# Performance work log

Hardware: AMD Instinct MI355X
Metric: run time of the kernel (lower is better)

Reference implementation:

```python
import jax, jax.numpy as jnp
import numpy as np

B, N_PER_G, H, K, A, GNN_STEPS = 64, 100, 64, 5, 50, 3
N = B * N_PER_G  # total nodes


def _lin(key, din, dout):
    s = 1.0 / np.sqrt(din)
    kw, kb = jax.random.split(key)
    w = jax.random.uniform(kw, (din, dout), minval=-s, maxval=s, dtype=jnp.float32)
    b = jax.random.uniform(kb, (dout,), minval=-s, maxval=s, dtype=jnp.float32)
    return w, b


def setup_inputs() -> dict:
    key = jax.random.key(0)
    ks = jax.random.split(key, 16)
    # complete graph (no self loops) per batch graph
    i, j = np.meshgrid(np.arange(N_PER_G), np.arange(N_PER_G), indexing="ij")
    m = i != j
    s0, d0 = i[m], j[m]  # [n*(n-1)]
    offs = (np.arange(B) * N_PER_G)[:, None]
    src = jnp.asarray((s0[None, :] + offs).reshape(-1), dtype=jnp.int32)
    dst = jnp.asarray((d0[None, :] + offs).reshape(-1), dtype=jnp.int32)
    E = src.shape[0]
    e_type = jax.random.uniform(ks[0], (E, 2), dtype=jnp.float32)
    d = jax.random.uniform(ks[1], (E, 1), dtype=jnp.float32)
    label = jax.nn.one_hot(jax.random.randint(ks[2], (N,), 0, K), K, dtype=jnp.float32)
    actions = jax.random.randint(ks[3], (B * A, 2), 0, N_PER_G)
    l1_w, l1_b = _lin(ks[4], K, H)
    l2_w, l2_b = _lin(ks[5], H, H)
    t3_w, t3_b = _lin(ks[6], H, H)
    t4_wf, t4_b = _lin(ks[7], 1, H)
    t5_wf, t5_b = _lin(ks[8], H, 1)
    t6_w, t6_b = _lin(ks[9], H, H)
    t7_1_w, t7_1_b = _lin(ks[10], H, H)
    t7_2_w, t7_2_b = _lin(ks[11], H, H)
    t9_1_w, t9_1_b = _lin(ks[12], H, H)
    t9_2_w, t9_2_b = _lin(ks[13], H, H)
    return dict(label=label, e_type=e_type, d=d,
                l1_w=l1_w, l1_b=l1_b, l2_w=l2_w, l2_b=l2_b,
                t3_w=t3_w, t3_b=t3_b, t4_w=t4_wf[0], t4_b=t4_b,
                t5_w=t5_wf[:, 0], t5_b=t5_b, t6_w=t6_w, t6_b=t6_b,
                t7_1_w=t7_1_w, t7_1_b=t7_1_b, t7_2_w=t7_2_w, t7_2_b=t7_2_b,
                t9_1_w=t9_1_w, t9_1_b=t9_1_b, t9_2_w=t9_2_w, t9_2_b=t9_2_b,
                src=src, dst=dst, actions=actions)


def reference(label, e_type, d, l1_w, l1_b, l2_w, l2_b, t3_w, t3_b, t4_w, t4_b,
              t5_w, t5_b, t6_w, t6_b, t7_1_w, t7_1_b, t7_2_w, t7_2_b,
              t9_1_w, t9_1_b, t9_2_w, t9_2_b, src, dst, actions):
    e1 = e_type[:, 0]
    # n1_hd = h[src]*e1, n1_d = d*e1; bmm(n1_hd^T, n1_d) == sum over in-edges of h[src]*e1^2*d
    w_e = (e1 * e1) * d[:, 0]                              # [E]
    s_e = d[:, 0] * e1                                     # per-edge n1_d scalar [E]
    # sum_deg relu(t4(n1_d)) as edge-parallel relu + scatter-add
    t4_edge = jax.nn.relu(s_e[:, None] * t4_w[None, :] + t4_b)   # [E,H]
    t4_sum = jax.ops.segment_sum(t4_edge, dst, num_segments=N)   # [N,H]
    base = label @ l1_w + l1_b + t4_sum @ t3_w + t3_b            # constant across gnn steps
    h = jnp.zeros((N, H), dtype=label.dtype)
    for _ in range(GNN_STEPS):
        n1_h = jax.ops.segment_sum(h[src] * w_e[:, None], dst, num_segments=N)  # [N,H]
        h = jax.nn.relu(base + n1_h @ l2_w + l2_b)
    # readout (forward_): graph mean -> t6 stem; per-action node-pair branch
    stem = h.reshape(B, N_PER_G, H).mean(axis=1) @ t6_w + t6_b    # [B,H]
    h2 = h @ t7_1_w + t7_1_b                                      # [N,H]
    offs = jnp.repeat(jnp.arange(B, dtype=actions.dtype) * N_PER_G, A)
    a = actions + offs[:, None]                                   # global node ids [B*A,2]
    ha = h2[a[:, 0]] + h2[a[:, 1]]                                # [B*A,H]
    u = jax.nn.relu(jax.nn.relu(ha) @ t7_2_w + t7_2_b) @ t9_2_w + t9_2_b
    g_branch = jax.nn.relu(stem) @ t9_1_w + t9_1_b                # [B,H]
    q = jax.nn.relu(g_branch[:, None, :] + u.reshape(B, A, H))    # [B,A,H]
    Q_sa = q.reshape(B * A, H) @ t5_w + t5_b[0]                   # [B*A]
    return Q_sa
```

## Files before the change

kernel.cpp:

```cpp
#include <hip/hip_runtime.h>

#define HD 64
#define NPG 100
#define NGRP 64
#define NACT 50
#define EPG 9900
#define HSTRIDE 409600
#define FLAGSTRIDE 4096
#define MAGICF 0x9E3779B9u

typedef const float* fcp;

#define ACC_CHUNK(CK)                                                         \
    for (int ib = 0; ib < 7; ++ib) {                                          \
        const float h0 = hs[((CK) * 28 + 4 * ib + 0) * HD + hh];              \
        const float h1 = hs[((CK) * 28 + 4 * ib + 1) * HD + hh];              \
        const float h2 = hs[((CK) * 28 + 4 * ib + 2) * HD + hh];              \
        const float h3 = hs[((CK) * 28 + 4 * ib + 3) * HD + hh];              \
        _Pragma("unroll")                                                     \
        for (int m = 0; m < 4; ++m) {                                         \
            const int jl = w + 8 * m;                                         \
            if (jl < 25) {                                                    \
                const float4 wv =                                             \
                    *(const float4*)&w_pad[jl * 112 + (CK) * 28 + 4 * ib];    \
                acc[m] += wv.x * h0 + wv.y * h1 + wv.z * h2 + wv.w * h3;      \
            }                                                                 \
        }                                                                     \
    }

__global__ __launch_bounds__(512)
void k_dqnet(fcp label, fcp e_type, fcp dvec,
             fcp l1_w, fcp l1_b, fcp l2_w, fcp l2_b,
             fcp t3_w, fcp t3_b, fcp t4_w, fcp t4_b,
             fcp t5_w, fcp t5_b, fcp t6_w, fcp t6_b,
             fcp t7_1_w, fcp t7_1_b, fcp t7_2_w, fcp t7_2_b,
             fcp t9_1_w, fcp t9_1_b, fcp t9_2_w, fcp t9_2_b,
             const int* __restrict__ actions,
             float* __restrict__ hstg, unsigned* __restrict__ flags,
             float* __restrict__ out)
{
    const int g  = blockIdx.x >> 2;
    const int c  = blockIdx.x & 3;
    const int j0 = c * 25;
    const int t  = threadIdx.x;
    const int hh = t & 63;
    const int w  = t >> 6;

    __shared__ __align__(16) float s_ld[2500];
    __shared__ __align__(16) float w_pad[25 * 112];
    __shared__ __align__(16) float hs[112 * HD];
    __shared__ __align__(16) float t4s[25 * HD];
    __shared__ __align__(16) float sh_l2w[HD * HD];
    __shared__ __align__(16) float sh_w71[HD * HD];
    __shared__ __align__(16) float sh_w72[HD * HD];
    __shared__ __align__(16) float sh_w92[HD * HD];
    __shared__ __align__(16) float awk[8 * HD];
    __shared__ float gbuf[HD];

    float l1r[5], lab[4][5];
    #pragma unroll
    for (int kk = 0; kk < 5; ++kk) l1r[kk] = l1_w[kk * HD + hh];
    #pragma unroll
    for (int m = 0; m < 4; ++m) {
        const int jl = w + 8 * m;
        #pragma unroll
        for (int kk = 0; kk < 5; ++kk)
            lab[m][kk] = (jl < 25) ? label[(g * NPG + j0 + jl) * 5 + kk] : 0.f;
    }
    const int acnt  = (c < 2) ? 13 : 12;
    const int abase = c * 12 + (c < 2 ? c : 2);
    int a0r[2], a1r[2];
    #pragma unroll
    for (int m = 0; m < 2; ++m) {
        const int al = w + 7 * m;
        a0r[m] = 0; a1r[m] = 0;
        if (w < 7 && al < acnt) {
            const int a = g * NACT + abase + al;
            a0r[m] = actions[a * 2 + 0];
            a1r[m] = actions[a * 2 + 1];
        }
        a0r[m] += 3 * (a0r[m] / 25);
        a1r[m] += 3 * (a1r[m] / 25);
    }

    for (int idx = t; idx < 768; idx += 512) {
        const int c2 = idx / 192, r = (idx % 192) / 64, ln = idx & 63;
        hs[(c2 * 28 + 25 + r) * HD + ln] = 0.f;
    }
    for (int idx = t; idx < 300; idx += 512) {
        const int jl = idx / 12, p = idx % 12;
        w_pad[jl * 112 + (p / 3) * 28 + 25 + (p % 3)] = 0.f;
    }

    const float2* et2 = (const float2*)e_type;
    const int ebase = g * EPG;
    for (int idx = t; idx < 2500; idx += 512) {
        const int i  = idx / 25;
        const int jl = idx - i * 25;
        const int j  = j0 + jl;
        float s = 0.f, wv = 0.f;
        if (i != j) {
            const int e = ebase + i * 99 + j - (j > i ? 1 : 0);
            const float e1 = et2[e].x;
            const float dd = dvec[e];
            s  = dd * e1;
            wv = e1 * e1 * dd;
        }
        s_ld[jl * 100 + i] = s;
        const int cb = i / 25;
        w_pad[jl * 112 + cb * 28 + (i - cb * 25)] = wv;
    }
    __syncthreads();

    const float w4  = t4_w[hh];
    const float b4  = t4_b[hh];
    const float rb4 = fmaxf(b4, 0.f);
    #pragma unroll
    for (int m = 0; m < 4; ++m) {
        const int jl = w + 8 * m;
        if (jl < 25) {
            float a0 = 0.f, a1 = 0.f, a2 = 0.f, a3 = 0.f;
            #pragma unroll 5
            for (int ib = 0; ib < 25; ++ib) {
                const float4 s4 = *(const float4*)&s_ld[jl * 100 + 4 * ib];
                a0 += fmaxf(s4.x * w4 + b4, 0.f);
                a1 += fmaxf(s4.y * w4 + b4, 0.f);
                a2 += fmaxf(s4.z * w4 + b4, 0.f);
                a3 += fmaxf(s4.w * w4 + b4, 0.f);
            }
            t4s[jl * HD + hh] = (a0 + a1) + (a2 + a3) - rb4;
        }
    }

    const float bb   = l1_b[hh] + t3_b[hh];
    const float l2bv = l2_b[hh];
    float basev[4];
    #pragma unroll
    for (int m = 0; m < 4; ++m) {
        float x = bb;
        #pragma unroll
        for (int kk = 0; kk < 5; ++kk) x += lab[m][kk] * l1r[kk];
        basev[m] = x;
    }
    for (int ib = 0; ib < 16; ++ib) {
        const float tw0 = t3_w[(4 * ib + 0) * HD + hh];
        const float tw1 = t3_w[(4 * ib + 1) * HD + hh];
        const float tw2 = t3_w[(4 * ib + 2) * HD + hh];
        const float tw3 = t3_w[(4 * ib + 3) * HD + hh];
        #pragma unroll
        for (int m = 0; m < 4; ++m) {
            const int jl = w + 8 * m;
            if (jl < 25) {
                const float4 x4 = *(const float4*)&t4s[jl * HD + 4 * ib];
                basev[m] += x4.x * tw0 + x4.y * tw1 + x4.z * tw2 + x4.w * tw3;
            }
        }
    }
    {
        #pragma unroll
        for (int m = 0; m < 4; ++m) {
            const int jl = w + 8 * m;
            if (jl < 25) {
                const float hv = fmaxf(basev[m] + l2bv, 0.f);
                hs[(c * 28 + jl) * HD + hh] = hv;
                __hip_atomic_store(hstg + (g * NPG + j0 + jl) * HD + hh, hv,
                                   __ATOMIC_RELAXED, __HIP_MEMORY_SCOPE_AGENT);
            }
        }
        asm volatile("s_waitcnt vmcnt(0)" ::: "memory");
        __syncthreads();
        if (t == 0)
            __hip_atomic_store(&flags[(g * 4 + c) * 16], MAGICF,
                               __ATOMIC_RELEASE, __HIP_MEMORY_SCOPE_AGENT);
    }

    {
        const float4* ls = (const float4*)l2_w;
        float4* ld = (float4*)sh_l2w;
        for (int idx = t; idx < 1024; idx += 512) ld[idx] = ls[idx];
        const float4* s71 = (const float4*)t7_1_w;
        float4* d71 = (float4*)sh_w71;
        for (int idx = t; idx < 1024; idx += 512) d71[idx] = s71[idx];
        const float4* s72 = (const float4*)t7_2_w;
        float4* d72 = (float4*)sh_w72;
        for (int idx = t; idx < 1024; idx += 512) d72[idx] = s72[idx];
        const float4* s92 = (const float4*)t9_2_w;
        float4* d92 = (float4*)sh_w92;
        for (int idx = t; idx < 1024; idx += 512) d92[idx] = s92[idx];
    }

    const int c1 = (c + 1) & 3, c2i = (c + 2) & 3, c3 = (c + 3) & 3;
    #pragma unroll 1
    for (int step = 0; step < 2; ++step) {
        const float* buf = hstg + step * HSTRIDE;
        unsigned* flg = flags + step * FLAGSTRIDE;
        float* bufn = hstg + (step + 1) * HSTRIDE;
        unsigned* flgn = flags + (step + 1) * FLAGSTRIDE;

        float acc[4];
        #pragma unroll
        for (int m = 0; m < 4; ++m) acc[m] = 0.f;

        ACC_CHUNK(c)

        if (t < 3) {
            const int cs = (c + 1 + t) & 3;
            while (__hip_atomic_load(&flg[(g * 4 + cs) * 16],
                                     __ATOMIC_RELAXED,
                                     __HIP_MEMORY_SCOPE_AGENT) != MAGICF)
                __builtin_amdgcn_s_sleep(1);
        }
        __syncthreads();

        const double* sb = (const double*)buf;
        const double* s1 = sb + (size_t)(g * NPG + c1 * 25) * 32;
        const double* s2 = sb + (size_t)(g * NPG + c2i * 25) * 32;
        const double* s3 = sb + (size_t)(g * NPG + c3 * 25) * 32;
        double* d1 = (double*)&hs[c1 * 28 * HD];
        double* d2 = (double*)&hs[c2i * 28 * HD];
        double* d3 = (double*)&hs[c3 * 28 * HD];
        const bool g2 = (t < 288);

        double a0 = __hip_atomic_load(s1 + t, __ATOMIC_RELAXED, __HIP_MEMORY_SCOPE_AGENT);
        double a1 = g2 ? __hip_atomic_load(s1 + 512 + t, __ATOMIC_RELAXED, __HIP_MEMORY_SCOPE_AGENT) : 0.0;
        double b0 = __hip_atomic_load(s2 + t, __ATOMIC_RELAXED, __HIP_MEMORY_SCOPE_AGENT);
        double b1 = g2 ? __hip_atomic_load(s2 + 512 + t, __ATOMIC_RELAXED, __HIP_MEMORY_SCOPE_AGENT) : 0.0;
        d1[t] = a0; if (g2) d1[512 + t] = a1;
        __syncthreads();
        double e0 = __hip_atomic_load(s3 + t, __ATOMIC_RELAXED, __HIP_MEMORY_SCOPE_AGENT);
        double e1 = g2 ? __hip_atomic_load(s3 + 512 + t, __ATOMIC_RELAXED, __HIP_MEMORY_SCOPE_AGENT) : 0.0;
        ACC_CHUNK(c1)
        d2[t] = b0; if (g2) d2[512 + t] = b1;
        __syncthreads();
        ACC_CHUNK(c2i)
        d3[t] = e0; if (g2) d3[512 + t] = e1;
        __syncthreads();
        ACC_CHUNK(c3)

        #pragma unroll
        for (int m = 0; m < 4; ++m) {
            const int jl = w + 8 * m;
            if (jl < 25) t4s[jl * HD + hh] = acc[m];
        }
        float v[4];
        #pragma unroll
        for (int m = 0; m < 4; ++m) v[m] = basev[m] + l2bv;
        for (int ib = 0; ib < 16; ++ib) {
            const float w0 = sh_l2w[(4 * ib + 0) * HD + hh];
            const float w1 = sh_l2w[(4 * ib + 1) * HD + hh];
            const float w2 = sh_l2w[(4 * ib + 2) * HD + hh];
            const float w3 = sh_l2w[(4 * ib + 3) * HD + hh];
            #pragma unroll
            for (int m = 0; m < 4; ++m) {
                const int jl = w + 8 * m;
                if (jl < 25) {
                    const float4 x4 = *(const float4*)&t4s[jl * HD + 4 * ib];
                    v[m] += x4.x * w0 + x4.y * w1 + x4.z * w2 + x4.w * w3;
                }
            }
        }
        #pragma unroll
        for (int m = 0; m < 4; ++m) {
            const int jl = w + 8 * m;
            if (jl < 25) {
                const float hv = fmaxf(v[m], 0.f);
                hs[(c * 28 + jl) * HD + hh] = hv;
                __hip_atomic_store(bufn + (g * NPG + j0 + jl) * HD + hh, hv,
                                   __ATOMIC_RELAXED, __HIP_MEMORY_SCOPE_AGENT);
            }
        }
        asm volatile("s_waitcnt vmcnt(0)" ::: "memory");
        __syncthreads();
        if (t == 0)
            __hip_atomic_store(&flgn[(g * 4 + c) * 16], MAGICF,
                               __ATOMIC_RELEASE, __HIP_MEMORY_SCOPE_AGENT);
    }

    {
        const float* buf2 = hstg + 2 * HSTRIDE;
        unsigned* flg2 = flags + 2 * FLAGSTRIDE;
        if (t < 3) {
            const int cs = (c + 1 + t) & 3;
            while (__hip_atomic_load(&flg2[(g * 4 + cs) * 16],
                                     __ATOMIC_RELAXED,
                                     __HIP_MEMORY_SCOPE_AGENT) != MAGICF)
                __builtin_amdgcn_s_sleep(1);
        }
        __syncthreads();
        const bool g2 = (t < 288);
        #pragma unroll
        for (int kk = 1; kk < 4; ++kk) {
            const int ck = (c + kk) & 3;
            const double* s = (const double*)buf2 + (size_t)(g * NPG + ck * 25) * 32;
            double* d = (double*)&hs[ck * 28 * HD];
            d[t] = __hip_atomic_load(s + t, __ATOMIC_RELAXED, __HIP_MEMORY_SCOPE_AGENT);
            if (g2) d[512 + t] = __hip_atomic_load(s + 512 + t, __ATOMIC_RELAXED, __HIP_MEMORY_SCOPE_AGENT);
        }
        __syncthreads();
    }

    {
        float ml = 0.f;
        for (int j = w; j < 112; j += 8) ml += hs[j * HD + hh];
        awk[w * HD + hh] = ml;
    }
    float* hsum = s_ld;
    float* r1s  = s_ld + 13 * HD;
    #pragma unroll
    for (int m = 0; m < 2; ++m) {
        const int al = w + 7 * m;
        if (w < 7 && al < acnt)
            hsum[al * HD + hh] = hs[a0r[m] * HD + hh] + hs[a1r[m] * HD + hh];
    }
    __syncthreads();

    if (w == 7) {
        float ml = 0.f;
        #pragma unroll
        for (int ww = 0; ww < 8; ++ww) ml += awk[ww * HD + hh];
        ml *= (1.f / NPG);
        float s = t6_b[hh];
        #pragma unroll 8
        for (int q = 0; q < HD; ++q) s += __shfl(ml, q, 64) * t6_w[q * HD + hh];
        s = fmaxf(s, 0.f);
        float gb = t9_1_b[hh];
        #pragma unroll 8
        for (int q = 0; q < HD; ++q) gb += __shfl(s, q, 64) * t9_1_w[q * HD + hh];
        gbuf[hh] = gb;
    } else {
        const float b71 = 2.f * t7_1_b[hh];
        float r[2];
        r[0] = b71; r[1] = b71;
        for (int ib = 0; ib < 16; ++ib) {
            const float w0 = sh_w71[(4 * ib + 0) * HD + hh];
            const float w1 = sh_w71[(4 * ib + 1) * HD + hh];
            const float w2 = sh_w71[(4 * ib + 2) * HD + hh];
            const float w3 = sh_w71[(4 * ib + 3) * HD + hh];
            #pragma unroll
            for (int m = 0; m < 2; ++m) {
                const int al = w + 7 * m;
                if (al < acnt) {
                    const float4 x4 = *(const float4*)&hsum[al * HD + 4 * ib];
                    r[m] += x4.x * w0 + x4.y * w1 + x4.z * w2 + x4.w * w3;
                }
            }
        }
        #pragma unroll
        for (int m = 0; m < 2; ++m) {
            const int al = w + 7 * m;
            if (al < acnt) r1s[al * HD + hh] = fmaxf(r[m], 0.f);
        }
        const float b72 = t7_2_b[hh];
        r[0] = b72; r[1] = b72;
        for (int ib = 0; ib < 16; ++ib) {
            const float w0 = sh_w72[(4 * ib + 0) * HD + hh];
            const float w1 = sh_w72[(4 * ib + 1) * HD + hh];
            const float w2 = sh_w72[(4 * ib + 2) * HD + hh];
            const float w3 = sh_w72[(4 * ib + 3) * HD + hh];
            #pragma unroll
            for (int m = 0; m < 2; ++m) {
                const int al = w + 7 * m;
                if (al < acnt) {
                    const float4 x4 = *(const float4*)&r1s[al * HD + 4 * ib];
                    r[m] += x4.x * w0 + x4.y * w1 + x4.z * w2 + x4.w * w3;
                }
            }
        }
        #pragma unroll
        for (int m = 0; m < 2; ++m) {
            const int al = w + 7 * m;
            if (al < acnt) hsum[al * HD + hh] = fmaxf(r[m], 0.f);
        }
    }
    __syncthreads();

    if (w < 7) {
        const float b92  = t9_2_b[hh];
        const float t5wv = t5_w[hh];
        const float t5bv = t5_b[0];
        const float gbv  = gbuf[hh];
        float u[2];
        u[0] = b92; u[1] = b92;
        for (int ib = 0; ib < 16; ++ib) {
            const float w0 = sh_w92[(4 * ib + 0) * HD + hh];
            const float w1 = sh_w92[(4 * ib + 1) * HD + hh];
            const float w2 = sh_w92[(4 * ib + 2) * HD + hh];
            const float w3 = sh_w92[(4 * ib + 3) * HD + hh];
            #pragma unroll
            for (int m = 0; m < 2; ++m) {
                const int al = w + 7 * m;
                if (al < acnt) {
                    const float4 x4 = *(const float4*)&hsum[al * HD + 4 * ib];
                    u[m] += x4.x * w0 + x4.y * w1 + x4.z * w2 + x4.w * w3;
                }
            }
        }
        #pragma unroll
        for (int m = 0; m < 2; ++m) {
            const int al = w + 7 * m;
            float qv = fmaxf(gbv + u[m], 0.f) * t5wv;
            #pragma unroll
            for (int off = 32; off > 0; off >>= 1) qv += __shfl_xor(qv, off, 64);
            if (al < acnt && hh == 0) out[g * NACT + abase + al] = qv + t5bv;
        }
    }
}

extern "C" void kernel_launch(void* const* d_in, const int* in_sizes, int n_in,
                              void* d_out, int out_size, void* d_ws, size_t ws_size,
                              hipStream_t stream)
{
    fcp label  = (fcp)d_in[0];
    fcp e_type = (fcp)d_in[1];
    fcp dvec   = (fcp)d_in[2];
    fcp l1_w   = (fcp)d_in[3];
    fcp l1_b   = (fcp)d_in[4];
    fcp l2_w   = (fcp)d_in[5];
    fcp l2_b   = (fcp)d_in[6];
    fcp t3_w   = (fcp)d_in[7];
    fcp t3_b   = (fcp)d_in[8];
    fcp t4_w   = (fcp)d_in[9];
    fcp t4_b   = (fcp)d_in[10];
    fcp t5_w   = (fcp)d_in[11];
    fcp t5_b   = (fcp)d_in[12];
    fcp t6_w   = (fcp)d_in[13];
    fcp t6_b   = (fcp)d_in[14];
    fcp t7_1_w = (fcp)d_in[15];
    fcp t7_1_b = (fcp)d_in[16];
    fcp t7_2_w = (fcp)d_in[17];
    fcp t7_2_b = (fcp)d_in[18];
    fcp t9_1_w = (fcp)d_in[19];
    fcp t9_1_b = (fcp)d_in[20];
    fcp t9_2_w = (fcp)d_in[21];
    fcp t9_2_b = (fcp)d_in[22];
    const int* actions = (const int*)d_in[25];

    char* ws = (char*)d_ws;
    float*    hstg  = (float*)ws;
    unsigned* flags = (unsigned*)(ws + 3 * 1638400);

    k_dqnet<<<dim3(NGRP * 4), dim3(512), 0, stream>>>(
        label, e_type, dvec, l1_w, l1_b, l2_w, l2_b, t3_w, t3_b, t4_w, t4_b,
        t5_w, t5_b, t6_w, t6_b, t7_1_w, t7_1_b, t7_2_w, t7_2_b,
        t9_1_w, t9_1_b, t9_2_w, t9_2_b, actions, hstg, flags, (float*)d_out);
}
```

Measured before the change: 157.1 us.

## Publish per-block partial node sums and gather only action rows after final step

After the last GNN step, each block no longer copies the three peer blocks' full hidden-state tiles into shared memory. Instead, every block writes a per-block partial sum of its node features to a new global psum buffer, which the readout warp combines for the graph mean. The action branch loads only the two needed node rows directly from the staged global buffer. This removes a large cross-block shared-memory reload and a barrier on the tail path, at the cost of extra flag-ordered global stores and scattered global loads.

```diff
diff --git a/kernel.cpp b/kernel.cpp
--- a/kernel.cpp
+++ b/kernel.cpp
@@ -37,6 +37,7 @@
              fcp t9_1_w, fcp t9_1_b, fcp t9_2_w, fcp t9_2_b,
              const int* __restrict__ actions,
              float* __restrict__ hstg, unsigned* __restrict__ flags,
+             float* __restrict__ psum,
              float* __restrict__ out)
 {
     const int g  = blockIdx.x >> 2;
@@ -79,8 +80,6 @@
             a0r[m] = actions[a * 2 + 0];
             a1r[m] = actions[a * 2 + 1];
         }
-        a0r[m] += 3 * (a0r[m] / 25);
-        a1r[m] += 3 * (a1r[m] / 25);
     }
 
     for (int idx = t; idx < 768; idx += 512) {
@@ -259,25 +258,38 @@
                 }
             }
         }
+        float psub = 0.f;
         #pragma unroll
         for (int m = 0; m < 4; ++m) {
             const int jl = w + 8 * m;
             if (jl < 25) {
                 const float hv = fmaxf(v[m], 0.f);
-                hs[(c * 28 + jl) * HD + hh] = hv;
+                if (step == 0) hs[(c * 28 + jl) * HD + hh] = hv;
+                psub += hv;
                 __hip_atomic_store(bufn + (g * NPG + j0 + jl) * HD + hh, hv,
                                    __ATOMIC_RELAXED, __HIP_MEMORY_SCOPE_AGENT);
             }
         }
+        if (step == 1) awk[w * HD + hh] = psub;
         asm volatile("s_waitcnt vmcnt(0)" ::: "memory");
         __syncthreads();
-        if (t == 0)
-            __hip_atomic_store(&flgn[(g * 4 + c) * 16], MAGICF,
-                               __ATOMIC_RELEASE, __HIP_MEMORY_SCOPE_AGENT);
-    }
-
+        if (w == 0) {
+            if (step == 1) {
+                float ps = 0.f;
+                #pragma unroll
+                for (int ww = 0; ww < 8; ++ww) ps += awk[ww * HD + hh];
+                __hip_atomic_store(psum + (g * 4 + c) * HD + hh, ps,
+                                   __ATOMIC_RELAXED, __HIP_MEMORY_SCOPE_AGENT);
+                asm volatile("s_waitcnt vmcnt(0)" ::: "memory");
+            }
+            if (hh == 0)
+                __hip_atomic_store(&flgn[(g * 4 + c) * 16], MAGICF,
+                                   __ATOMIC_RELEASE, __HIP_MEMORY_SCOPE_AGENT);
+        }
+    }
+
+    const float* buf2 = hstg + 2 * HSTRIDE;
     {
-        const float* buf2 = hstg + 2 * HSTRIDE;
         unsigned* flg2 = flags + 2 * FLAGSTRIDE;
         if (t < 3) {
             const int cs = (c + 1 + t) & 3;
@@ -287,37 +299,16 @@
                 __builtin_amdgcn_s_sleep(1);
         }
         __syncthreads();
-        const bool g2 = (t < 288);
-        #pragma unroll
-        for (int kk = 1; kk < 4; ++kk) {
-            const int ck = (c + kk) & 3;
-            const double* s = (const double*)buf2 + (size_t)(g * NPG + ck * 25) * 32;
-            double* d = (double*)&hs[ck * 28 * HD];
-            d[t] = __hip_atomic_load(s + t, __ATOMIC_RELAXED, __HIP_MEMORY_SCOPE_AGENT);
-            if (g2) d[512 + t] = __hip_atomic_load(s + 512 + t, __ATOMIC_RELAXED, __HIP_MEMORY_SCOPE_AGENT);
-        }
-        __syncthreads();
-    }
-
-    {
-        float ml = 0.f;
-        for (int j = w; j < 112; j += 8) ml += hs[j * HD + hh];
-        awk[w * HD + hh] = ml;
-    }
+    }
+
     float* hsum = s_ld;
     float* r1s  = s_ld + 13 * HD;
-    #pragma unroll
-    for (int m = 0; m < 2; ++m) {
-        const int al = w + 7 * m;
-        if (w < 7 && al < acnt)
-            hsum[al * HD + hh] = hs[a0r[m] * HD + hh] + hs[a1r[m] * HD + hh];
-    }
-    __syncthreads();
-
     if (w == 7) {
         float ml = 0.f;
         #pragma unroll
-        for (int ww = 0; ww < 8; ++ww) ml += awk[ww * HD + hh];
+        for (int cc = 0; cc < 4; ++cc)
+            ml += __hip_atomic_load(psum + (g * 4 + cc) * HD + hh,
+                                    __ATOMIC_RELAXED, __HIP_MEMORY_SCOPE_AGENT);
         ml *= (1.f / NPG);
         float s = t6_b[hh];
         #pragma unroll 8
@@ -328,6 +319,26 @@
         for (int q = 0; q < HD; ++q) gb += __shfl(s, q, 64) * t9_1_w[q * HD + hh];
         gbuf[hh] = gb;
     } else {
+        float ha[2];
+        #pragma unroll
+        for (int m = 0; m < 2; ++m) {
+            const int al = w + 7 * m;
+            ha[m] = 0.f;
+            if (al < acnt) {
+                const float v0 = __hip_atomic_load(
+                    buf2 + (g * NPG + a0r[m]) * HD + hh,
+                    __ATOMIC_RELAXED, __HIP_MEMORY_SCOPE_AGENT);
+                const float v1 = __hip_atomic_load(
+                    buf2 + (g * NPG + a1r[m]) * HD + hh,
+                    __ATOMIC_RELAXED, __HIP_MEMORY_SCOPE_AGENT);
+                ha[m] = v0 + v1;
+            }
+        }
+        #pragma unroll
+        for (int m = 0; m < 2; ++m) {
+            const int al = w + 7 * m;
+            if (al < acnt) hsum[al * HD + hh] = ha[m];
+        }
         const float b71 = 2.f * t7_1_b[hh];
         float r[2];
         r[0] = b71; r[1] = b71;
@@ -438,9 +449,11 @@
     char* ws = (char*)d_ws;
     float*    hstg  = (float*)ws;
     unsigned* flags = (unsigned*)(ws + 3 * 1638400);
+    float*    psum  = (float*)(ws + 3 * 1638400 + 3 * FLAGSTRIDE * 4);
 
     k_dqnet<<<dim3(NGRP * 4), dim3(512), 0, stream>>>(
         label, e_type, dvec, l1_w, l1_b, l2_w, l2_b, t3_w, t3_b, t4_w, t4_b,
         t5_w, t5_b, t6_w, t6_b, t7_1_w, t7_1_b, t7_2_w, t7_2_b,
-        t9_1_w, t9_1_b, t9_2_w, t9_2_b, actions, hstg, flags, (float*)d_out);
+        t9_1_w, t9_1_b, t9_2_w, t9_2_b, actions, hstg, flags, psum,
+        (float*)d_out);
 }
```

Result: no change. 156.1 us (-0.6%).
